# Performance work log

Hardware: AMD Instinct MI355X
Metric: run time of the kernel (lower is better)

## Reference

```python
import jax, jax.numpy as jnp
from jax import lax
import numpy as np

HID = 128; NRAD = 32; NAZ = 8; EPS_BN = 1e-5

def _bn(x, p):
    # p: [4, C] = (gamma, beta, running_mean, running_var); eval-mode batchnorm
    g, b, m, v = p
    sh = (1, -1) + (1,) * (x.ndim - 2)
    return (x - m.reshape(sh)) * (g.reshape(sh) / jnp.sqrt(v.reshape(sh) + EPS_BN)) + b.reshape(sh)

def _conv2d(x, w, b):
    y = lax.conv_general_dilated(x, w, (1, 1), 'SAME', dimension_numbers=('NCHW', 'OIHW', 'NCHW'))
    return y + b.reshape(1, -1, 1, 1)

def _conv1d(x, w, b):
    y = lax.conv_general_dilated(x, w, (1,), 'SAME', dimension_numbers=('NCH', 'OIH', 'NCH'))
    return y + b.reshape(1, -1, 1)

def setup_inputs():
    key = jax.random.key(0)
    ks = iter(jax.random.split(key, 48))
    def W(shape, s=0.05):
        return jax.random.normal(next(ks), shape, jnp.float32) * s
    def bias(c):
        return jax.random.normal(next(ks), (c,), jnp.float32) * 0.01
    def bn(c):
        g = 1.0 + 0.1 * jax.random.normal(next(ks), (c,), jnp.float32)
        b = 0.1 * jax.random.normal(next(ks), (c,), jnp.float32)
        m = 0.05 * jax.random.normal(next(ks), (c,), jnp.float32)
        v = 0.5 + jax.random.uniform(next(ks), (c,), jnp.float32)
        return jnp.stack([g, b, m, v])
    B, C, H, Wd = 16, 3, 256, 256
    h2, h4 = HID // 2, HID // 4
    comb = h2 + h4 + h4 + NAZ * C * 2  # 64+32+32+48 = 176
    return {
        'x': jax.random.normal(next(ks), (B, C, H, Wd), jnp.float32),
        'mw1': W((h2, C, 3, 3)), 'mb1': bias(h2), 'mbn1': bn(h2),
        'mw2': W((h2, h2, 3, 3)), 'mb2': bias(h2), 'mbn2': bn(h2),
        'pw1': W((h4, C, 3, 3)), 'pb1': bias(h4), 'pbn1': bn(h4),
        'pw2': W((h4, h4, 3, 3)), 'pb2': bias(h4), 'pbn2': bn(h4),
        'rw1': W((h4, C, 3)), 'rb1': bias(h4), 'rbn1': bn(h4),
        'rw2': W((h4, h4, 3)), 'rb2': bias(h4), 'rbn2': bn(h4),
        'lw1': W((HID * 2, comb)), 'lb1': bias(HID * 2),
        'lng': jnp.ones((HID * 2,), jnp.float32), 'lnb': jnp.zeros((HID * 2,), jnp.float32),
        'lw2': W((HID, HID * 2)), 'lb2': bias(HID),
    }

def _forward(x, mw1, mb1, mbn1, mw2, mb2, mbn2, pw1, pb1, pbn1, pw2, pb2, pbn2,
             rw1, rb1, rbn1, rw2, rb2, rbn2, lw1, lb1, lng, lnb, lw2, lb2):
    B, C, H, Wd = x.shape
    xf = jnp.clip(x.astype(jnp.float32), -10.0, 10.0)
    freq = jnp.fft.rfft2(xf, axes=(-2, -1))                         # [B,C,H,W//2+1] complex
    mag = jnp.clip(jnp.abs(freq), 1e-8, 1e6)
    mag_log = jnp.clip(jnp.log1p(mag), -20.0, 20.0)
    phase = jnp.clip(jnp.angle(freq) / np.pi, -1.0, 1.0)

    # static frequency-grid bin indices
    fy = jnp.fft.fftfreq(H).astype(jnp.float32)
    fx = jnp.fft.rfftfreq(Wd).astype(jnp.float32)
    fyg, fxg = jnp.meshgrid(fy, fx, indexing='ij')
    radius = jnp.sqrt(fxg ** 2 + fyg ** 2)
    rbins = jnp.clip((radius / (radius.max() + 1e-8) * (NRAD - 1)).astype(jnp.int32), 0, NRAD - 1).reshape(-1)
    angle = jnp.arctan2(fyg, fxg + 1e-8)
    abins = jnp.clip(((angle + np.pi) / (2 * np.pi) * NAZ).astype(jnp.int32), 0, NAZ - 1).reshape(-1)

    mag_flat = mag.reshape(B, C, -1)                                # [B,C,N]
    # radial power spectrum: segment mean via one-hot contraction
    r_oh = jax.nn.one_hot(rbins, NRAD, dtype=jnp.float32)           # [N,NRAD]
    r_cnt = jnp.maximum(r_oh.sum(0), 1.0)
    radial = jnp.clip(jnp.einsum('bcn,nk->bck', mag_flat, r_oh) / r_cnt, 0.0, 1e6)  # [B,C,NRAD]

    # azimuthal mean / unbiased std per angular sector (single pass sum/sumsq/count)
    a_oh = jax.nn.one_hot(abins, NAZ, dtype=jnp.float32)            # [N,NAZ]
    a_cnt = a_oh.sum(0)
    s1 = jnp.einsum('bcn,nk->bck', mag_flat, a_oh)
    s2 = jnp.einsum('bcn,nk->bck', mag_flat ** 2, a_oh)
    a_mean = s1 / a_cnt
    a_var = (s2 - a_cnt * a_mean ** 2) / jnp.maximum(a_cnt - 1.0, 1.0)
    a_std = jnp.sqrt(jnp.maximum(a_var, 0.0))
    # torch cat order: mean_bin0, std_bin0, mean_bin1, std_bin1, ... each [B,C]
    az = jnp.stack([a_mean.transpose(0, 2, 1), a_std.transpose(0, 2, 1)], axis=2).reshape(B, NAZ * 2 * C)
    az = jnp.nan_to_num(az, nan=0.0, posinf=1e4, neginf=-1e4)

    # bilinear upsample to (H,W); jax.image.resize uses half-pixel centers == align_corners=False
    mag_sp = jax.image.resize(mag_log, (B, C, H, Wd), 'bilinear')
    ph_sp = jax.image.resize(phase, (B, C, H, Wd), 'bilinear')

    mag_feat = jax.nn.relu(_bn(_conv2d(mag_sp, mw1, mb1), mbn1))
    mag_feat = jax.nn.relu(_bn(_conv2d(mag_feat, mw2, mb2), mbn2))
    mag_pool = mag_feat.mean((2, 3))
    ph_feat = jax.nn.relu(_bn(_conv2d(ph_sp, pw1, pb1), pbn1))
    ph_feat = jax.nn.relu(_bn(_conv2d(ph_feat, pw2, pb2), pbn2))
    ph_pool = ph_feat.mean((2, 3))

    rf = jax.nn.relu(_bn(_conv1d(radial, rw1, rb1), rbn1))
    rf = jax.nn.relu(_bn(_conv1d(rf, rw2, rb2), rbn2))
    rf = rf.mean(-1)                                                # AdaptiveAvgPool1d(1)+Flatten

    comb = jnp.concatenate([mag_pool, ph_pool, rf, az], axis=1)    # [B,176]
    comb = jnp.nan_to_num(comb, nan=0.0, posinf=1e4, neginf=-1e4)
    h = comb @ lw1.T + lb1
    mu = h.mean(-1, keepdims=True)
    var = ((h - mu) ** 2).mean(-1, keepdims=True)
    h = (h - mu) / jnp.sqrt(var + 1e-5) * lng + lnb                 # LayerNorm
    h = jax.nn.relu(h)                                              # dropout = identity (eval)
    out = h @ lw2.T + lb2
    out = jnp.clip(out, -100.0, 100.0)
    return jnp.nan_to_num(out, nan=0.0, posinf=100.0, neginf=-100.0)

def reference(x, mw1, mb1, mbn1, mw2, mb2, mbn2, pw1, pb1, pbn1, pw2, pb2, pbn2,
              rw1, rb1, rbn1, rw2, rb2, rbn2, lw1, lb1, lng, lnb, lw2, lb2):
    return _forward(x, mw1, mb1, mbn1, mw2, mb2, mbn2, pw1, pb1, pbn1, pw2, pb2, pbn2,
                    rw1, rb1, rbn1, rw2, rb2, rbn2, lw1, lb1, lng, lnb, lw2, lb2)
```

## Files before the change

### kernel.cpp

```cpp
#include <hip/hip_runtime.h>
#include <math.h>

#define PI_F 3.14159274101257324f
#define TWO_PI_256 0.02454369260617026f
#define TWO_PI_16  0.39269908169872414f

typedef __attribute__((ext_vector_type(8))) short bf16x8;
typedef __attribute__((ext_vector_type(4))) float f32x4;

static const size_t OFF_FC    = 0;
static const size_t OFF_MLOG  = 3170304;
static const size_t OFF_PH    = 4755456;
static const size_t OFF_RSUM  = 9486336;
static const size_t OFF_RCNT  = OFF_RSUM + 1536;
static const size_t OFF_AS1   = OFF_RCNT + 32;
static const size_t OFF_AS2   = OFF_AS1 + 384;
static const size_t OFF_ACNT  = OFF_AS2 + 384;
static const size_t OFF_MPOOL = OFF_ACNT + 8;
static const size_t OFF_PPOOL = OFF_MPOOL + 1024;
static const size_t OFF_RF    = OFF_PPOOL + 512;
static const size_t OFF_PAR   = OFF_RF + 512;
static const size_t OFF_WBM   = OFF_PAR + 512;
static const size_t OFF_WBP   = OFF_WBM + 18432;
static const size_t OFF_W1BM  = OFF_WBP + 4608;
static const size_t OFF_W1BP  = OFF_W1BM + 1024;

__device__ __forceinline__ float fix_nan(float v, float pinf, float ninf) {
  if (isnan(v)) return 0.f;
  if (isinf(v)) return v > 0.f ? pinf : ninf;
  return v;
}

__device__ __forceinline__ unsigned short f2bf(float f) {
  unsigned u = __float_as_uint(f);
  unsigned r = (u + 0x7FFFu + ((u >> 16) & 1u)) >> 16;
  return (unsigned short)r;
}

__device__ __forceinline__ void fold_bn(const float* bn, int C, int c, float cb,
                                        float* s, float* t) {
  float g = bn[c], b = bn[C + c], m = bn[2 * C + c], v = bn[3 * C + c];
  float sc = g / sqrtf(v + 1e-5f);
  *s = sc;
  *t = b + (cb - m) * sc;
}

__global__ __launch_bounds__(256) void row_fft_prep(
    const float* __restrict__ x, float* __restrict__ Fc, float* __restrict__ zbuf,
    const float* __restrict__ mw1, const float* __restrict__ pw1,
    const float* __restrict__ mw2, const float* __restrict__ pw2,
    const float* __restrict__ mb1, const float* __restrict__ mbn1,
    const float* __restrict__ mb2, const float* __restrict__ mbn2,
    const float* __restrict__ pb1, const float* __restrict__ pbn1,
    const float* __restrict__ pb2, const float* __restrict__ pbn2,
    const float* __restrict__ rb1, const float* __restrict__ rbn1,
    const float* __restrict__ rb2, const float* __restrict__ rbn2,
    float* __restrict__ par, unsigned short* __restrict__ wbm,
    unsigned short* __restrict__ wbp, unsigned short* __restrict__ w1bm,
    unsigned short* __restrict__ w1bp) {
  const int blk = blockIdx.x;
  const int tid = threadIdx.x;
  if (blk >= 12288) {
    int idx = (blk - 12288) * 256 + tid;
    if (idx < 36864) {
      int pos = idx / 4096, rem = idx % 4096;
      int oc = rem >> 6, ci = rem & 63;
      wbm[idx] = f2bf(mw2[(oc * 64 + ci) * 9 + pos]);
    } else if (idx < 46080) {
      int i = idx - 36864;
      int pos = i / 1024, rem = i % 1024;
      int oc = rem >> 5, ci = rem & 31;
      wbp[i] = f2bf(pw2[(oc * 32 + ci) * 9 + pos]);
    } else if (idx < 46336) {
      int i = idx - 46080;
      float s, t;
      if (i < 64)       { fold_bn(mbn1, 64, i, mb1[i], &s, &t);          par[i] = s;       par[64 + i] = t; }
      else if (i < 128) { int c = i - 64;  fold_bn(mbn2, 64, c, mb2[c], &s, &t); par[128 + c] = s; par[192 + c] = t; }
      else if (i < 160) { int c = i - 128; fold_bn(pbn1, 32, c, pb1[c], &s, &t); par[256 + c] = s; par[288 + c] = t; }
      else if (i < 192) { int c = i - 160; fold_bn(pbn2, 32, c, pb2[c], &s, &t); par[320 + c] = s; par[352 + c] = t; }
      else if (i < 224) { int c = i - 192; fold_bn(rbn1, 32, c, rb1[c], &s, &t); par[384 + c] = s; par[416 + c] = t; }
      else              { int c = i - 224; fold_bn(rbn2, 32, c, rb2[c], &s, &t); par[448 + c] = s; par[480 + c] = t; }
    } else if (idx < 48384) {
      int i = idx - 46336;
      int oc = i >> 5, k = i & 31;
      w1bm[i] = (k < 27) ? f2bf(mw1[oc * 27 + k]) : (unsigned short)0;
    } else if (idx < 49408) {
      int i = idx - 48384;
      int oc = i >> 5, k = i & 31;
      w1bp[i] = (k < 27) ? f2bf(pw1[oc * 27 + k]) : (unsigned short)0;
    }
    return;
  }
  if (blk == 0) {
    for (int i = tid; i < 3880; i += 256) zbuf[i] = 0.f;
  }
  __shared__ float xr[256];
  __shared__ float2 sS[256];
  {
    float v = x[(size_t)blk * 256 + tid];
    xr[tid] = fminf(fmaxf(v, -10.f), 10.f);
  }
  __syncthreads();
  {
    int b16 = tid >> 4, m = tid & 15;
    float sW, cW;
    sincosf(TWO_PI_16 * (float)m, &sW, &cW);
    float sr = 0.f, si = 0.f, wr = 1.f, wi = 0.f;
#pragma unroll
    for (int a = 0; a < 16; ++a) {
      float xv = xr[a * 16 + b16];
      sr = fmaf(xv, wr, sr);
      si = fmaf(xv, wi, si);
      float nr = wr * cW + wi * sW;
      float ni = wi * cW - wr * sW;
      wr = nr; wi = ni;
    }
    sS[b16 * 16 + m] = make_float2(sr, si);
  }
  __syncthreads();
  if (tid < 129) {
    int m2 = tid & 15;
    float sK, cK;
    sincosf(TWO_PI_256 * (float)tid, &sK, &cK);
    float fr = 0.f, fi = 0.f, wr = 1.f, wi = 0.f;
#pragma unroll
    for (int bb = 0; bb < 16; ++bb) {
      float2 s = sS[bb * 16 + m2];
      fr = fmaf(s.x, wr, fr); fr = fmaf(-s.y, wi, fr);
      fi = fmaf(s.x, wi, fi); fi = fmaf(s.y, wr, fi);
      float nr = wr * cK + wi * sK;
      float ni = wi * cK - wr * sK;
      wr = nr; wi = ni;
    }
    float2* o = (float2*)Fc;
    o[(size_t)blk * 129 + tid] = make_float2(fr, fi);
  }
}

__global__ __launch_bounds__(256) void col_fft_stats(
    const float* __restrict__ Fc, float* __restrict__ mlog, float* __restrict__ ph,
    float* __restrict__ rsum, float* __restrict__ rcnt, float* __restrict__ as1,
    float* __restrict__ as2, float* __restrict__ acnt) {
  const int k = blockIdx.x, b = blockIdx.y;
  const int tid = threadIdx.x;
  const int cp = tid >> 7;
  __shared__ float2 col[3][256];
  __shared__ float2 sS[3][256];
  __shared__ float l_rs[3][2][32];
  __shared__ float l_rc[32];
  __shared__ float l_s1[3][2][8], l_s2[3][2][8];
  __shared__ float l_ac[8];
  for (int i = tid; i < 192; i += 256) {
    int c = i / 64, r = i % 64;
    l_rs[c][r >> 5][r & 31] = 0.f;
  }
  if (tid < 32) l_rc[tid] = 0.f;
  if (tid < 48) { int c = tid / 16, r = tid % 16; l_s1[c][r >> 3][r & 7] = 0.f; l_s2[c][r >> 3][r & 7] = 0.f; }
  if (tid < 8) l_ac[tid] = 0.f;
  const float2* fc = (const float2*)Fc;
#pragma unroll
  for (int c = 0; c < 3; ++c)
    col[c][tid] = fc[((size_t)((b * 3 + c) * 256) + tid) * 129 + k];
  __syncthreads();
  {
    int b16 = tid >> 4, m = tid & 15;
    float sW, cW;
    sincosf(TWO_PI_16 * (float)m, &sW, &cW);
#pragma unroll
    for (int c = 0; c < 3; ++c) {
      float sr = 0.f, si = 0.f, wr = 1.f, wi = 0.f;
#pragma unroll
      for (int a = 0; a < 16; ++a) {
        float2 v = col[c][a * 16 + b16];
        sr = fmaf(v.x, wr, sr); sr = fmaf(-v.y, wi, sr);
        si = fmaf(v.x, wi, si); si = fmaf(v.y, wr, si);
        float nr = wr * cW + wi * sW;
        float ni = wi * cW - wr * sW;
        wr = nr; wi = ni;
      }
      sS[c][b16 * 16 + m] = make_float2(sr, si);
    }
  }
  __syncthreads();
  const int j = tid;
  float sK, cK;
  sincosf(TWO_PI_256 * (float)j, &sK, &cK);
  float gr[3], gi[3];
#pragma unroll
  for (int c = 0; c < 3; ++c) {
    float fr = 0.f, fi = 0.f, wr = 1.f, wi = 0.f;
#pragma unroll
    for (int bb = 0; bb < 16; ++bb) {
      float2 s = sS[c][bb * 16 + (j & 15)];
      fr = fmaf(s.x, wr, fr); fr = fmaf(-s.y, wi, fr);
      fi = fmaf(s.x, wi, fi); fi = fmaf(s.y, wr, fi);
      float nr = wr * cK + wi * sK;
      float ni = wi * cK - wr * sK;
      wr = nr; wi = ni;
    }
    gr[c] = fr; gi[c] = fi;
  }
  float fy = (float)(j < 128 ? j : j - 256) * (1.0f / 256.0f);
  float fx = (float)k * (1.0f / 256.0f);
  float rad = sqrtf(fx * fx + fy * fy);
  float denom = sqrtf(0.5f) + 1e-8f;
  int rb = (int)((rad / denom) * 31.0f);
  rb = rb < 0 ? 0 : (rb > 31 ? 31 : rb);
  float ang = atan2f(fy, fx + 1e-8f);
  int ab = (int)((ang + PI_F) / (2.0f * PI_F) * 8.0f);
  ab = ab < 0 ? 0 : (ab > 7 ? 7 : ab);
#pragma unroll
  for (int c = 0; c < 3; ++c) {
    float mag = sqrtf(gr[c] * gr[c] + gi[c] * gi[c]);
    mag = fminf(fmaxf(mag, 1e-8f), 1e6f);
    float ml = fminf(fmaxf(log1pf(mag), -20.f), 20.f);
    float p = fminf(fmaxf(atan2f(gi[c], gr[c]) / PI_F, -1.f), 1.f);
    size_t oidx = ((size_t)((b * 3 + c) * 256) + j) * 129 + k;
    mlog[oidx] = ml;
    ph[oidx] = p;
    atomicAdd(&l_rs[c][cp][rb], mag);
    atomicAdd(&l_s1[c][cp][ab], mag);
    atomicAdd(&l_s2[c][cp][ab], mag * mag);
  }
  if (b == 0) {
    atomicAdd(&l_rc[rb], 1.0f);
    atomicAdd(&l_ac[ab], 1.0f);
  }
  __syncthreads();
  if (tid < 96) {
    int c = tid / 32, i2 = tid % 32;
    atomicAdd(&rsum[(b * 3 + c) * 32 + i2], l_rs[c][0][i2] + l_rs[c][1][i2]);
  } else if (tid < 120) {
    int t2 = tid - 96;
    int c = t2 / 8, a2 = t2 % 8;
    atomicAdd(&as1[(b * 3 + c) * 8 + a2], l_s1[c][0][a2] + l_s1[c][1][a2]);
    atomicAdd(&as2[(b * 3 + c) * 8 + a2], l_s2[c][0][a2] + l_s2[c][1][a2]);
  }
  if (b == 0) {
    if (tid < 32) atomicAdd(&rcnt[tid], l_rc[tid]);
    else if (tid < 40) atomicAdd(&acnt[tid - 32], l_ac[tid - 32]);
  }
}

template <int C2>
__global__ __launch_bounds__(256, 2) void conv_mfma(
    const float* __restrict__ src,
    const unsigned short* __restrict__ w1b,
    const unsigned short* __restrict__ wB,
    const float* __restrict__ s1, const float* __restrict__ t1,
    const float* __restrict__ s2, const float* __restrict__ t2,
    float* __restrict__ pool) {
  constexpr int ST = C2 + 8;
  constexpr int NT = C2 / 16;
  constexpr int WNT = (C2 == 64) ? 2 : 1;
  constexpr int KS = C2 / 32;
  constexpr int NG = 3 * KS;

  __shared__ float s_in[3][20][20];
  __shared__ float s_sc1[C2], s_sh1[C2];
  __shared__ __align__(16) unsigned short s_f1[324 * ST];

  const int tid = threadIdx.x;
  const int b = blockIdx.z;
  const int tx0 = blockIdx.x * 16, ty0 = blockIdx.y * 16;
  const int lane = tid & 63, wv = tid >> 6;
  const int ln = lane & 15, q = lane >> 4;
  const int ntg = wv & 1, half = wv >> 1;
  const int ocb0 = ntg * WNT * 16;

  for (int idx = tid; idx < 1200; idx += 256) {
    int c = idx / 400, r = idx % 400, iy = r / 20, ix = r % 20;
    int gy = ty0 - 2 + iy, gx = tx0 - 2 + ix;
    float v = 0.f;
    if ((unsigned)gy < 256u && (unsigned)gx < 256u) {
      float srcx = ((float)gx + 0.5f) * (129.0f / 256.0f) - 0.5f;
      float fl = floorf(srcx);
      float w = srcx - fl;
      int x0 = (int)fl, x1 = x0 + 1;
      x0 = x0 < 0 ? 0 : x0;
      x1 = x1 > 128 ? 128 : x1;
      const float* rowp = src + ((size_t)(b * 3 + c) * 256 + gy) * 129;
      v = rowp[x0] * (1.f - w) + rowp[x1] * w;
    }
    s_in[c][iy][ix] = v;
  }
  if (tid < C2) { s_sc1[tid] = s1[tid]; s_sh1[tid] = t1[tid]; }

  bf16x8 b1[NT];
#pragma unroll
  for (int nt = 0; nt < NT; ++nt)
    b1[nt] = *(const bf16x8*)&w1b[(nt * 16 + ln) * 32 + q * 8];

  bf16x8 Bb[2][3 * WNT];
  bf16x8 Bw[(C2 == 32) ? 9 : 1];
  if constexpr (C2 == 64) {
#pragma unroll
    for (int ky = 0; ky < 3; ++ky)
#pragma unroll
      for (int w = 0; w < 2; ++w)
        Bb[0][ky * 2 + w] =
            *(const bf16x8*)&wB[((size_t)(ky * 3) * 64 + ocb0 + w * 16 + ln) * 64 + q * 8];
  } else {
#pragma unroll
    for (int kx = 0; kx < 3; ++kx)
#pragma unroll
      for (int ky = 0; ky < 3; ++ky)
        Bw[kx * 3 + ky] =
            *(const bf16x8*)&wB[((size_t)(ky * 3 + kx) * 32 + ocb0 + ln) * 32 + q * 8];
  }

  __syncthreads();

  float c1sc[NT][4], c1sh[NT][4];
#pragma unroll
  for (int nt = 0; nt < NT; ++nt)
#pragma unroll
    for (int r = 0; r < 4; ++r) {
      c1sc[nt][r] = s_sc1[nt * 16 + q * 4 + r];
      c1sh[nt][r] = s_sh1[nt * 16 + q * 4 + r];
    }

  const float* sp = &s_in[0][0][0];
  int koff[8];
#pragma unroll
  for (int j = 0; j < 8; ++j) {
    int k = q * 8 + j;
    if (k < 27) {
      int c = k / 9, rr = k - c * 9, dy = rr / 3, dx = rr - dy * 3;
      koff[j] = (c * 20 + dy) * 20 + dx;
    } else koff[j] = -1;
  }
  for (int mt = wv; mt < 21; mt += 4) {
    int p = mt * 16 + ln;
    int pc = p < 324 ? p : 0;
    int py = pc / 18, px = pc - py * 18;
    int pix = py * 20 + px;
    union { bf16x8 v; unsigned u[4]; } af;
#pragma unroll
    for (int jj = 0; jj < 4; ++jj) {
      float v0 = (koff[2 * jj] >= 0) ? sp[koff[2 * jj] + pix] : 0.f;
      float v1 = (koff[2 * jj + 1] >= 0) ? sp[koff[2 * jj + 1] + pix] : 0.f;
      af.u[jj] = (unsigned)f2bf(v0) | ((unsigned)f2bf(v1) << 16);
    }
    bool inim = false;
    if (p < 324) {
      int gy = ty0 - 1 + py, gx = tx0 - 1 + px;
      inim = ((unsigned)gy < 256u) && ((unsigned)gx < 256u);
    }
#pragma unroll
    for (int nt = 0; nt < NT; ++nt) {
      f32x4 c1 = __builtin_amdgcn_mfma_f32_16x16x32_bf16(
          b1[nt], af.v, (f32x4){0.f, 0.f, 0.f, 0.f}, 0, 0, 0);
      if (p < 324) {
        float v0 = inim ? fmaxf(fmaf(c1[0], c1sc[nt][0], c1sh[nt][0]), 0.f) : 0.f;
        float v1 = inim ? fmaxf(fmaf(c1[1], c1sc[nt][1], c1sh[nt][1]), 0.f) : 0.f;
        float v2 = inim ? fmaxf(fmaf(c1[2], c1sc[nt][2], c1sh[nt][2]), 0.f) : 0.f;
        float v3 = inim ? fmaxf(fmaf(c1[3], c1sc[nt][3], c1sh[nt][3]), 0.f) : 0.f;
        uint2 pk;
        pk.x = (unsigned)f2bf(v0) | ((unsigned)f2bf(v1) << 16);
        pk.y = (unsigned)f2bf(v2) | ((unsigned)f2bf(v3) << 16);
        *(uint2*)&s_f1[p * ST + nt * 16 + q * 4] = pk;
      }
    }
  }
  __syncthreads();

  f32x4 acc[WNT][8];
#pragma unroll
  for (int w = 0; w < WNT; ++w)
#pragma unroll
    for (int i = 0; i < 8; ++i)
      acc[w][i] = (f32x4){0.f, 0.f, 0.f, 0.f};

  const int rbase = half * 8;
#pragma unroll
  for (int g = 0; g < NG; ++g) {
    const int kx = g / KS, ks = g % KS;
    if constexpr (C2 == 64) {
      if (g + 1 < NG) {
        const int nkx = (g + 1) / KS, nks = (g + 1) % KS;
#pragma unroll
        for (int ky = 0; ky < 3; ++ky)
#pragma unroll
          for (int w = 0; w < 2; ++w)
            Bb[(g + 1) & 1][ky * 2 + w] =
                *(const bf16x8*)&wB[((size_t)(ky * 3 + nkx) * 64 + ocb0 + w * 16 + ln) * 64 +
                                    nks * 32 + q * 8];
      }
    }
    bf16x8 a[10];
#pragma unroll
    for (int rr = 0; rr < 10; ++rr)
      a[rr] = *(const bf16x8*)&s_f1[((rbase + rr) * 18 + ln + kx) * ST + ks * 32 + q * 8];
#pragma unroll
    for (int ky = 0; ky < 3; ++ky)
#pragma unroll
      for (int w = 0; w < WNT; ++w) {
        bf16x8 bf;
        if constexpr (C2 == 64) bf = Bb[g & 1][ky * 2 + w];
        else bf = Bw[kx * 3 + ky];
#pragma unroll
        for (int i = 0; i < 8; ++i)
          acc[w][i] = __builtin_amdgcn_mfma_f32_16x16x32_bf16(a[i + ky], bf, acc[w][i], 0, 0, 0);
      }
  }

#pragma unroll
  for (int w = 0; w < WNT; ++w) {
    const int oc = ocb0 + w * 16 + ln;
    const float sc = s2[oc], sh = t2[oc];
    float v = 0.f;
#pragma unroll
    for (int i = 0; i < 8; ++i)
#pragma unroll
      for (int r = 0; r < 4; ++r)
        v += fmaxf(fmaf(acc[w][i][r], sc, sh), 0.f);
    v += __shfl_xor(v, 16);
    v += __shfl_xor(v, 32);
    if (q == 0) atomicAdd(&pool[b * C2 + oc], v);
  }
}

__global__ __launch_bounds__(256) void final_mlp(
    const float* __restrict__ rsum, const float* __restrict__ rcnt,
    const float* __restrict__ rw1, const float* __restrict__ rw2,
    const float* __restrict__ sr1, const float* __restrict__ tr1,
    const float* __restrict__ sr2, const float* __restrict__ tr2,
    const float* __restrict__ mpool, const float* __restrict__ ppool,
    const float* __restrict__ as1, const float* __restrict__ as2,
    const float* __restrict__ acnt,
    const float* __restrict__ lw1, const float* __restrict__ lb1,
    const float* __restrict__ lng, const float* __restrict__ lnb,
    const float* __restrict__ lw2, const float* __restrict__ lb2,
    float* __restrict__ out) {
  int b = blockIdx.x, t = threadIdx.x;
  __shared__ float rad[3][32];
  __shared__ float rf1[32][32];
  __shared__ float rf2[32][32];
  __shared__ float rfv[32];
  __shared__ float comb[176];
  __shared__ float red[256];
  __shared__ float hrelu[256];
  __shared__ float s_mu, s_var;

  if (t < 96) {
    int c = t / 32, i = t % 32;
    float cnt = fmaxf(rcnt[i], 1.0f);
    float v = rsum[(b * 3 + c) * 32 + i] / cnt;
    rad[c][i] = fminf(fmaxf(v, 0.f), 1e6f);
  }
  __syncthreads();
  for (int idx = t; idx < 1024; idx += 256) {
    int oc = idx >> 5, i = idx & 31;
    float a = 0.f;
    for (int c = 0; c < 3; ++c)
#pragma unroll
      for (int d = 0; d < 3; ++d) {
        int ii = i + d - 1;
        if (ii >= 0 && ii < 32) a = fmaf(rad[c][ii], rw1[(oc * 3 + c) * 3 + d], a);
      }
    rf1[oc][i] = fmaxf(fmaf(a, sr1[oc], tr1[oc]), 0.f);
  }
  __syncthreads();
  for (int idx = t; idx < 1024; idx += 256) {
    int oc = idx >> 5, i = idx & 31;
    float a = 0.f;
    for (int c = 0; c < 32; ++c)
#pragma unroll
      for (int d = 0; d < 3; ++d) {
        int ii = i + d - 1;
        if (ii >= 0 && ii < 32) a = fmaf(rf1[c][ii], rw2[(oc * 32 + c) * 3 + d], a);
      }
    rf2[oc][i] = fmaxf(fmaf(a, sr2[oc], tr2[oc]), 0.f);
  }
  __syncthreads();
  if (t < 32) {
    float s = 0.f;
    for (int i = 0; i < 32; ++i) s += rf2[t][i];
    rfv[t] = s * (1.0f / 32.0f);
  }
  __syncthreads();

  if (t < 64) comb[t] = fix_nan(mpool[b * 64 + t] * (1.0f / 65536.0f), 1e4f, -1e4f);
  else if (t < 96) comb[t] = fix_nan(ppool[b * 32 + t - 64] * (1.0f / 65536.0f), 1e4f, -1e4f);
  else if (t < 128) comb[t] = fix_nan(rfv[t - 96], 1e4f, -1e4f);
  else if (t < 176) {
    int j = t - 128;
    int a = j / 6, r = j % 6, m = r / 3, c = r % 3;
    float cnt = acnt[a];
    float v = 0.f;
    if (cnt > 0.f) {
      float s1v = as1[(b * 3 + c) * 8 + a], s2v = as2[(b * 3 + c) * 8 + a];
      float mean = s1v / cnt;
      if (m == 0)
        v = mean;
      else {
        float var = (s2v - cnt * mean * mean) / fmaxf(cnt - 1.f, 1.f);
        v = sqrtf(fmaxf(var, 0.f));
      }
    }
    comb[t] = fix_nan(v, 1e4f, -1e4f);
  }
  __syncthreads();
  float h = lb1[t];
  const float* wr = lw1 + t * 176;
#pragma unroll 8
  for (int j = 0; j < 176; ++j) h = fmaf(comb[j], wr[j], h);
  red[t] = h;
  __syncthreads();
  for (int s = 128; s > 0; s >>= 1) {
    if (t < s) red[t] += red[t + s];
    __syncthreads();
  }
  if (t == 0) s_mu = red[0] * (1.0f / 256.0f);
  __syncthreads();
  float mu = s_mu;
  float d = h - mu;
  red[t] = d * d;
  __syncthreads();
  for (int s = 128; s > 0; s >>= 1) {
    if (t < s) red[t] += red[t + s];
    __syncthreads();
  }
  if (t == 0) s_var = red[0] * (1.0f / 256.0f);
  __syncthreads();
  float hn = d / sqrtf(s_var + 1e-5f) * lng[t] + lnb[t];
  hrelu[t] = fmaxf(hn, 0.f);
  __syncthreads();
  if (t < 128) {
    float o = lb2[t];
    const float* w2r = lw2 + t * 256;
#pragma unroll 8
    for (int j = 0; j < 256; ++j) o = fmaf(hrelu[j], w2r[j], o);
    o = fminf(fmaxf(o, -100.f), 100.f);
    out[b * 128 + t] = fix_nan(o, 100.f, -100.f);
  }
}

extern "C" void kernel_launch(void* const* d_in, const int* in_sizes, int n_in,
                              void* d_out, int out_size, void* d_ws, size_t ws_size,
                              hipStream_t stream) {
  const float* x    = (const float*)d_in[0];
  const float* mw1  = (const float*)d_in[1];
  const float* mb1  = (const float*)d_in[2];
  const float* mbn1 = (const float*)d_in[3];
  const float* mw2  = (const float*)d_in[4];
  const float* mb2  = (const float*)d_in[5];
  const float* mbn2 = (const float*)d_in[6];
  const float* pw1  = (const float*)d_in[7];
  const float* pb1  = (const float*)d_in[8];
  const float* pbn1 = (const float*)d_in[9];
  const float* pw2  = (const float*)d_in[10];
  const float* pb2  = (const float*)d_in[11];
  const float* pbn2 = (const float*)d_in[12];
  const float* rw1  = (const float*)d_in[13];
  const float* rb1  = (const float*)d_in[14];
  const float* rbn1 = (const float*)d_in[15];
  const float* rw2  = (const float*)d_in[16];
  const float* rb2  = (const float*)d_in[17];
  const float* rbn2 = (const float*)d_in[18];
  const float* lw1  = (const float*)d_in[19];
  const float* lb1  = (const float*)d_in[20];
  const float* lng  = (const float*)d_in[21];
  const float* lnb  = (const float*)d_in[22];
  const float* lw2  = (const float*)d_in[23];
  const float* lb2  = (const float*)d_in[24];

  float* ws = (float*)d_ws;
  float* out = (float*)d_out;

  float* fc    = ws + OFF_FC;
  float* mlog  = ws + OFF_MLOG;
  float* phb   = ws + OFF_PH;
  float* rsum  = ws + OFF_RSUM;
  float* rcnt  = ws + OFF_RCNT;
  float* as1   = ws + OFF_AS1;
  float* as2   = ws + OFF_AS2;
  float* acnt  = ws + OFF_ACNT;
  float* mpool = ws + OFF_MPOOL;
  float* ppool = ws + OFF_PPOOL;
  float* par   = ws + OFF_PAR;
  unsigned short* wbm  = (unsigned short*)(ws + OFF_WBM);
  unsigned short* wbp  = (unsigned short*)(ws + OFF_WBP);
  unsigned short* w1bm = (unsigned short*)(ws + OFF_W1BM);
  unsigned short* w1bp = (unsigned short*)(ws + OFF_W1BP);

  row_fft_prep<<<12481, 256, 0, stream>>>(x, fc, rsum,
                                          mw1, pw1, mw2, pw2, mb1, mbn1, mb2, mbn2,
                                          pb1, pbn1, pb2, pbn2, rb1, rbn1, rb2, rbn2,
                                          par, wbm, wbp, w1bm, w1bp);
  col_fft_stats<<<dim3(129, 16), 256, 0, stream>>>(fc, mlog, phb, rsum, rcnt,
                                                   as1, as2, acnt);
  conv_mfma<64><<<dim3(16, 16, 16), 256, 0, stream>>>(
      mlog, w1bm, wbm, par + 0, par + 64, par + 128, par + 192, mpool);
  conv_mfma<32><<<dim3(16, 16, 16), 256, 0, stream>>>(
      phb, w1bp, wbp, par + 256, par + 288, par + 320, par + 352, ppool);
  final_mlp<<<16, 256, 0, stream>>>(rsum, rcnt, rw1, rw2, par + 384, par + 416,
                                    par + 448, par + 480, mpool, ppool, as1, as2,
                                    acnt, lw1, lb1, lng, lnb, lw2, lb2, out);
}
```

Before: 443.2 us.

## Batch two rows per FFT block and four columns per column-FFT block

The row FFT kernel now processes two image rows per block, sharing twiddle recurrences and halving the block count. The column FFT kernel is regridded so each block handles one channel and four adjacent frequency columns. This makes the strided gather of Fc fetch neighbouring columns together and reuses the twiddle computation across them. The final MLP dot products are split into four independent accumulators to shorten FMA dependency chains. Idle threads in the last column group and the changed summation order are minor side effects.

```diff
diff --git a/kernel.cpp b/kernel.cpp
--- a/kernel.cpp
+++ b/kernel.cpp
@@ -60,8 +60,8 @@
     unsigned short* __restrict__ w1bp) {
   const int blk = blockIdx.x;
   const int tid = threadIdx.x;
-  if (blk >= 12288) {
-    int idx = (blk - 12288) * 256 + tid;
+  if (blk >= 6144) {
+    int idx = (blk - 6144) * 256 + tid;
     if (idx < 36864) {
       int pos = idx / 4096, rem = idx % 4096;
       int oc = rem >> 6, ci = rem & 63;
@@ -94,46 +94,55 @@
   if (blk == 0) {
     for (int i = tid; i < 3880; i += 256) zbuf[i] = 0.f;
   }
-  __shared__ float xr[256];
-  __shared__ float2 sS[256];
-  {
-    float v = x[(size_t)blk * 256 + tid];
-    xr[tid] = fminf(fmaxf(v, -10.f), 10.f);
+  __shared__ float xr[2][256];
+  __shared__ float2 sS[2][256];
+  for (int i = tid; i < 512; i += 256) {
+    int rw = i >> 8, w = i & 255;
+    float v = x[((size_t)blk * 2 + rw) * 256 + w];
+    xr[rw][w] = fminf(fmaxf(v, -10.f), 10.f);
   }
   __syncthreads();
   {
     int b16 = tid >> 4, m = tid & 15;
     float sW, cW;
     sincosf(TWO_PI_16 * (float)m, &sW, &cW);
-    float sr = 0.f, si = 0.f, wr = 1.f, wi = 0.f;
+    float sr0 = 0.f, si0 = 0.f, sr1 = 0.f, si1 = 0.f, wr = 1.f, wi = 0.f;
 #pragma unroll
     for (int a = 0; a < 16; ++a) {
-      float xv = xr[a * 16 + b16];
-      sr = fmaf(xv, wr, sr);
-      si = fmaf(xv, wi, si);
+      float x0 = xr[0][a * 16 + b16];
+      float x1 = xr[1][a * 16 + b16];
+      sr0 = fmaf(x0, wr, sr0);
+      si0 = fmaf(x0, wi, si0);
+      sr1 = fmaf(x1, wr, sr1);
+      si1 = fmaf(x1, wi, si1);
       float nr = wr * cW + wi * sW;
       float ni = wi * cW - wr * sW;
       wr = nr; wi = ni;
     }
-    sS[b16 * 16 + m] = make_float2(sr, si);
+    sS[0][b16 * 16 + m] = make_float2(sr0, si0);
+    sS[1][b16 * 16 + m] = make_float2(sr1, si1);
   }
   __syncthreads();
   if (tid < 129) {
     int m2 = tid & 15;
     float sK, cK;
     sincosf(TWO_PI_256 * (float)tid, &sK, &cK);
-    float fr = 0.f, fi = 0.f, wr = 1.f, wi = 0.f;
+    float fr0 = 0.f, fi0 = 0.f, fr1 = 0.f, fi1 = 0.f, wr = 1.f, wi = 0.f;
 #pragma unroll
     for (int bb = 0; bb < 16; ++bb) {
-      float2 s = sS[bb * 16 + m2];
-      fr = fmaf(s.x, wr, fr); fr = fmaf(-s.y, wi, fr);
-      fi = fmaf(s.x, wi, fi); fi = fmaf(s.y, wr, fi);
+      float2 s0 = sS[0][bb * 16 + m2];
+      float2 s1 = sS[1][bb * 16 + m2];
+      fr0 = fmaf(s0.x, wr, fr0); fr0 = fmaf(-s0.y, wi, fr0);
+      fi0 = fmaf(s0.x, wi, fi0); fi0 = fmaf(s0.y, wr, fi0);
+      fr1 = fmaf(s1.x, wr, fr1); fr1 = fmaf(-s1.y, wi, fr1);
+      fi1 = fmaf(s1.x, wi, fi1); fi1 = fmaf(s1.y, wr, fi1);
       float nr = wr * cK + wi * sK;
       float ni = wi * cK - wr * sK;
       wr = nr; wi = ni;
     }
     float2* o = (float2*)Fc;
-    o[(size_t)blk * 129 + tid] = make_float2(fr, fi);
+    o[((size_t)blk * 2 + 0) * 129 + tid] = make_float2(fr0, fi0);
+    o[((size_t)blk * 2 + 1) * 129 + tid] = make_float2(fr1, fi1);
   }
 }
 
@@ -141,102 +150,111 @@
     const float* __restrict__ Fc, float* __restrict__ mlog, float* __restrict__ ph,
     float* __restrict__ rsum, float* __restrict__ rcnt, float* __restrict__ as1,
     float* __restrict__ as2, float* __restrict__ acnt) {
-  const int k = blockIdx.x, b = blockIdx.y;
+  const int kg = blockIdx.x;
+  const int b  = blockIdx.y;
+  const int c  = blockIdx.z;
+  const int bc = b * 3 + c;
   const int tid = threadIdx.x;
   const int cp = tid >> 7;
-  __shared__ float2 col[3][256];
-  __shared__ float2 sS[3][256];
-  __shared__ float l_rs[3][2][32];
+  const int k0 = kg * 4;
+  __shared__ float2 colt[4][256];
+  __shared__ float2 sSt[4][256];
+  __shared__ float l_rs[2][32];
   __shared__ float l_rc[32];
-  __shared__ float l_s1[3][2][8], l_s2[3][2][8];
+  __shared__ float l_s1[2][8], l_s2[2][8];
   __shared__ float l_ac[8];
-  for (int i = tid; i < 192; i += 256) {
-    int c = i / 64, r = i % 64;
-    l_rs[c][r >> 5][r & 31] = 0.f;
-  }
+  if (tid < 64) l_rs[tid >> 5][tid & 31] = 0.f;
   if (tid < 32) l_rc[tid] = 0.f;
-  if (tid < 48) { int c = tid / 16, r = tid % 16; l_s1[c][r >> 3][r & 7] = 0.f; l_s2[c][r >> 3][r & 7] = 0.f; }
+  if (tid < 16) { l_s1[tid >> 3][tid & 7] = 0.f; l_s2[tid >> 3][tid & 7] = 0.f; }
   if (tid < 8) l_ac[tid] = 0.f;
   const float2* fc = (const float2*)Fc;
-#pragma unroll
-  for (int c = 0; c < 3; ++c)
-    col[c][tid] = fc[((size_t)((b * 3 + c) * 256) + tid) * 129 + k];
+  for (int idx = tid; idx < 1024; idx += 256) {
+    int y = idx >> 2, kk = idx & 3;
+    int k = k0 + kk;
+    k = k > 128 ? 128 : k;
+    colt[kk][y] = fc[((size_t)(bc * 256) + y) * 129 + k];
+  }
   __syncthreads();
   {
     int b16 = tid >> 4, m = tid & 15;
     float sW, cW;
     sincosf(TWO_PI_16 * (float)m, &sW, &cW);
-#pragma unroll
-    for (int c = 0; c < 3; ++c) {
-      float sr = 0.f, si = 0.f, wr = 1.f, wi = 0.f;
-#pragma unroll
-      for (int a = 0; a < 16; ++a) {
-        float2 v = col[c][a * 16 + b16];
-        sr = fmaf(v.x, wr, sr); sr = fmaf(-v.y, wi, sr);
-        si = fmaf(v.x, wi, si); si = fmaf(v.y, wr, si);
-        float nr = wr * cW + wi * sW;
-        float ni = wi * cW - wr * sW;
-        wr = nr; wi = ni;
-      }
-      sS[c][b16 * 16 + m] = make_float2(sr, si);
-    }
+    float sr[4] = {0.f, 0.f, 0.f, 0.f}, si[4] = {0.f, 0.f, 0.f, 0.f};
+    float wr = 1.f, wi = 0.f;
+#pragma unroll
+    for (int a = 0; a < 16; ++a) {
+#pragma unroll
+      for (int kk = 0; kk < 4; ++kk) {
+        float2 v = colt[kk][a * 16 + b16];
+        sr[kk] = fmaf(v.x, wr, sr[kk]); sr[kk] = fmaf(-v.y, wi, sr[kk]);
+        si[kk] = fmaf(v.x, wi, si[kk]); si[kk] = fmaf(v.y, wr, si[kk]);
+      }
+      float nr = wr * cW + wi * sW;
+      float ni = wi * cW - wr * sW;
+      wr = nr; wi = ni;
+    }
+#pragma unroll
+    for (int kk = 0; kk < 4; ++kk)
+      sSt[kk][b16 * 16 + m] = make_float2(sr[kk], si[kk]);
   }
   __syncthreads();
   const int j = tid;
   float sK, cK;
   sincosf(TWO_PI_256 * (float)j, &sK, &cK);
-  float gr[3], gi[3];
-#pragma unroll
-  for (int c = 0; c < 3; ++c) {
-    float fr = 0.f, fi = 0.f, wr = 1.f, wi = 0.f;
+  float gr[4] = {0.f, 0.f, 0.f, 0.f}, gi[4] = {0.f, 0.f, 0.f, 0.f};
+  {
+    const int m2 = j & 15;
+    float wr = 1.f, wi = 0.f;
 #pragma unroll
     for (int bb = 0; bb < 16; ++bb) {
-      float2 s = sS[c][bb * 16 + (j & 15)];
-      fr = fmaf(s.x, wr, fr); fr = fmaf(-s.y, wi, fr);
-      fi = fmaf(s.x, wi, fi); fi = fmaf(s.y, wr, fi);
+#pragma unroll
+      for (int kk = 0; kk < 4; ++kk) {
+        float2 s = sSt[kk][bb * 16 + m2];
+        gr[kk] = fmaf(s.x, wr, gr[kk]); gr[kk] = fmaf(-s.y, wi, gr[kk]);
+        gi[kk] = fmaf(s.x, wi, gi[kk]); gi[kk] = fmaf(s.y, wr, gi[kk]);
+      }
       float nr = wr * cK + wi * sK;
       float ni = wi * cK - wr * sK;
       wr = nr; wi = ni;
     }
-    gr[c] = fr; gi[c] = fi;
   }
   float fy = (float)(j < 128 ? j : j - 256) * (1.0f / 256.0f);
-  float fx = (float)k * (1.0f / 256.0f);
-  float rad = sqrtf(fx * fx + fy * fy);
-  float denom = sqrtf(0.5f) + 1e-8f;
-  int rb = (int)((rad / denom) * 31.0f);
-  rb = rb < 0 ? 0 : (rb > 31 ? 31 : rb);
-  float ang = atan2f(fy, fx + 1e-8f);
-  int ab = (int)((ang + PI_F) / (2.0f * PI_F) * 8.0f);
-  ab = ab < 0 ? 0 : (ab > 7 ? 7 : ab);
-#pragma unroll
-  for (int c = 0; c < 3; ++c) {
-    float mag = sqrtf(gr[c] * gr[c] + gi[c] * gi[c]);
+  const float denom = sqrtf(0.5f) + 1e-8f;
+#pragma unroll
+  for (int kk = 0; kk < 4; ++kk) {
+    int k = k0 + kk;
+    if (k > 128) break;
+    float fx = (float)k * (1.0f / 256.0f);
+    float rad = sqrtf(fx * fx + fy * fy);
+    int rb = (int)((rad / denom) * 31.0f);
+    rb = rb < 0 ? 0 : (rb > 31 ? 31 : rb);
+    float ang = atan2f(fy, fx + 1e-8f);
+    int ab = (int)((ang + PI_F) / (2.0f * PI_F) * 8.0f);
+    ab = ab < 0 ? 0 : (ab > 7 ? 7 : ab);
+    float mag = sqrtf(gr[kk] * gr[kk] + gi[kk] * gi[kk]);
     mag = fminf(fmaxf(mag, 1e-8f), 1e6f);
     float ml = fminf(fmaxf(log1pf(mag), -20.f), 20.f);
-    float p = fminf(fmaxf(atan2f(gi[c], gr[c]) / PI_F, -1.f), 1.f);
-    size_t oidx = ((size_t)((b * 3 + c) * 256) + j) * 129 + k;
+    float p = fminf(fmaxf(atan2f(gi[kk], gr[kk]) / PI_F, -1.f), 1.f);
+    size_t oidx = ((size_t)(bc * 256) + j) * 129 + k;
     mlog[oidx] = ml;
     ph[oidx] = p;
-    atomicAdd(&l_rs[c][cp][rb], mag);
-    atomicAdd(&l_s1[c][cp][ab], mag);
-    atomicAdd(&l_s2[c][cp][ab], mag * mag);
-  }
-  if (b == 0) {
-    atomicAdd(&l_rc[rb], 1.0f);
-    atomicAdd(&l_ac[ab], 1.0f);
-  }
-  __syncthreads();
-  if (tid < 96) {
-    int c = tid / 32, i2 = tid % 32;
-    atomicAdd(&rsum[(b * 3 + c) * 32 + i2], l_rs[c][0][i2] + l_rs[c][1][i2]);
-  } else if (tid < 120) {
-    int t2 = tid - 96;
-    int c = t2 / 8, a2 = t2 % 8;
-    atomicAdd(&as1[(b * 3 + c) * 8 + a2], l_s1[c][0][a2] + l_s1[c][1][a2]);
-    atomicAdd(&as2[(b * 3 + c) * 8 + a2], l_s2[c][0][a2] + l_s2[c][1][a2]);
-  }
-  if (b == 0) {
+    atomicAdd(&l_rs[cp][rb], mag);
+    atomicAdd(&l_s1[cp][ab], mag);
+    atomicAdd(&l_s2[cp][ab], mag * mag);
+    if (b == 0 && c == 0) {
+      atomicAdd(&l_rc[rb], 1.0f);
+      atomicAdd(&l_ac[ab], 1.0f);
+    }
+  }
+  __syncthreads();
+  if (tid < 32) {
+    atomicAdd(&rsum[bc * 32 + tid], l_rs[0][tid] + l_rs[1][tid]);
+  } else if (tid < 40) {
+    int a = tid - 32;
+    atomicAdd(&as1[bc * 8 + a], l_s1[0][a] + l_s1[1][a]);
+    atomicAdd(&as2[bc * 8 + a], l_s2[0][a] + l_s2[1][a]);
+  }
+  if (b == 0 && c == 0) {
     if (tid < 32) atomicAdd(&rcnt[tid], l_rc[tid]);
     else if (tid < 40) atomicAdd(&acnt[tid - 32], l_ac[tid - 32]);
   }
@@ -502,10 +520,16 @@
     comb[t] = fix_nan(v, 1e4f, -1e4f);
   }
   __syncthreads();
-  float h = lb1[t];
   const float* wr = lw1 + t * 176;
-#pragma unroll 8
-  for (int j = 0; j < 176; ++j) h = fmaf(comb[j], wr[j], h);
+  float h0 = 0.f, h1 = 0.f, h2 = 0.f, h3 = 0.f;
+#pragma unroll 4
+  for (int j = 0; j < 176; j += 4) {
+    h0 = fmaf(comb[j], wr[j], h0);
+    h1 = fmaf(comb[j + 1], wr[j + 1], h1);
+    h2 = fmaf(comb[j + 2], wr[j + 2], h2);
+    h3 = fmaf(comb[j + 3], wr[j + 3], h3);
+  }
+  float h = lb1[t] + ((h0 + h1) + (h2 + h3));
   red[t] = h;
   __syncthreads();
   for (int s = 128; s > 0; s >>= 1) {
@@ -528,10 +552,16 @@
   hrelu[t] = fmaxf(hn, 0.f);
   __syncthreads();
   if (t < 128) {
-    float o = lb2[t];
     const float* w2r = lw2 + t * 256;
-#pragma unroll 8
-    for (int j = 0; j < 256; ++j) o = fmaf(hrelu[j], w2r[j], o);
+    float o0 = 0.f, o1 = 0.f, o2 = 0.f, o3 = 0.f;
+#pragma unroll 4
+    for (int j = 0; j < 256; j += 4) {
+      o0 = fmaf(hrelu[j], w2r[j], o0);
+      o1 = fmaf(hrelu[j + 1], w2r[j + 1], o1);
+      o2 = fmaf(hrelu[j + 2], w2r[j + 2], o2);
+      o3 = fmaf(hrelu[j + 3], w2r[j + 3], o3);
+    }
+    float o = lb2[t] + ((o0 + o1) + (o2 + o3));
     o = fminf(fmaxf(o, -100.f), 100.f);
     out[b * 128 + t] = fix_nan(o, 100.f, -100.f);
   }
@@ -585,12 +615,12 @@
   unsigned short* w1bm = (unsigned short*)(ws + OFF_W1BM);
   unsigned short* w1bp = (unsigned short*)(ws + OFF_W1BP);
 
-  row_fft_prep<<<12481, 256, 0, stream>>>(x, fc, rsum,
-                                          mw1, pw1, mw2, pw2, mb1, mbn1, mb2, mbn2,
-                                          pb1, pbn1, pb2, pbn2, rb1, rbn1, rb2, rbn2,
-                                          par, wbm, wbp, w1bm, w1bp);
-  col_fft_stats<<<dim3(129, 16), 256, 0, stream>>>(fc, mlog, phb, rsum, rcnt,
-                                                   as1, as2, acnt);
+  row_fft_prep<<<6337, 256, 0, stream>>>(x, fc, rsum,
+                                         mw1, pw1, mw2, pw2, mb1, mbn1, mb2, mbn2,
+                                         pb1, pbn1, pb2, pbn2, rb1, rbn1, rb2, rbn2,
+                                         par, wbm, wbp, w1bm, w1bp);
+  col_fft_stats<<<dim3(33, 16, 3), 256, 0, stream>>>(fc, mlog, phb, rsum, rcnt,
+                                                     as1, as2, acnt);
   conv_mfma<64><<<dim3(16, 16, 16), 256, 0, stream>>>(
       mlog, w1bm, wbm, par + 0, par + 64, par + 128, par + 192, mpool);
   conv_mfma<32><<<dim3(16, 16, 16), 256, 0, stream>>>(
```

After: 435.8 us. No clear change (-1.7%).
